# Optimization experiments

Measured on AMD Instinct MI355X. Metric: run time of the kernel, lower is better.

The kernel has to match this reference:

```python
import jax, jax.numpy as jnp
import numpy as np

B, H, N, D = 1, 8, 2048, 64  # n >> d: fastmax's intended long-seq / small-head-dim regime


def setup_inputs() -> dict:
    key = jax.random.key(0)
    kq, kk, kv, kr = jax.random.split(key, 4)
    q = jax.random.normal(kq, (B, H, N, D), dtype=jnp.float32)
    k = jax.random.normal(kk, (B, H, N, D), dtype=jnp.float32)
    v = jax.random.normal(kv, (B, H, N, D), dtype=jnp.float32)
    rpe_matrix = jax.random.normal(kr, (2 * N - 1, D), dtype=jnp.float32)
    return {"q": q, "k": k, "v": v, "rpe_matrix": rpe_matrix, "mask": 1}


def reference(q, k, v, rpe_matrix, mask):
    # Fastmax: 2nd-order Taylor approximation of softmax attention,
    # weight(i,j) = 1 + s_ij + s_ij^2 / 2 where s_ij = q_i . (k_j) + q_i . rpe[i-j+n-1],
    # normalized by the row-sum, optionally causal (mask).
    b, h, n, d = q.shape
    # content scores: (b,h,n,n)
    s = jnp.einsum('bhid,bhjd->bhij', q, k)
    # RPE scores: project q onto every relative-position embedding, then gather
    # the (i,j) -> i-j+n-1 diagonal structure.  qr: (b,h,n,2n-1)
    qr = jnp.einsum('bhid,md->bhim', q, rpe_matrix)
    i = jnp.arange(n)[:, None]
    j = jnp.arange(n)[None, :]
    rel = i - j + (n - 1)  # (n,n) in [0, 2n-2]
    s = s + jnp.take_along_axis(qr, rel[None, None], axis=-1)
    # Taylor-2 exp approximation
    w = 1.0 + s + 0.5 * s * s
    if mask:  # causal
        w = jnp.where(j <= i, w, 0.0)
    denom = jnp.sum(w, axis=-1, keepdims=True)  # (b,h,n,1)
    out = jnp.einsum('bhij,bhjd->bhid', w, v) / denom
    return out
```

## Files before the change

kernel.cpp:

```cpp
#include <hip/hip_runtime.h>
#include <hip/hip_bf16.h>

#define HH 8
#define NN 2048
#define DD 64

typedef __attribute__((ext_vector_type(8))) short bf16x8;
typedef __attribute__((ext_vector_type(4))) float f32x4;
typedef __attribute__((ext_vector_type(8))) unsigned short u16x8;
typedef unsigned short ushort_t;

static __device__ __forceinline__ unsigned short f2bf(float x) {
    union { float f; unsigned u; } un; un.f = x;
    unsigned r = un.u + 0x7FFFu + ((un.u >> 16) & 1u);
    return (unsigned short)(r >> 16);
}

#define OFF_Q  0u
#define OFF_K  2097152u
#define OFF_VT 4194304u
#define OFF_R  6291456u
#define OFF_P  6815744u
#define WS_NEED 11272192u

#define NQ4 262144
#define NR4 65520
__global__ void cvt_kernel(const float* __restrict__ q, const float* __restrict__ k,
                           const float* __restrict__ r, ushort_t* __restrict__ ws) {
    int idx = blockIdx.x * 256 + threadIdx.x;
    const float* src; ushort_t* dst; int off;
    if (idx < NQ4) { src = q; dst = (ushort_t*)((char*)ws + OFF_Q); off = idx; }
    else if (idx < 2 * NQ4) { src = k; dst = (ushort_t*)((char*)ws + OFF_K); off = idx - NQ4; }
    else if (idx < 2 * NQ4 + NR4) { src = r; dst = (ushort_t*)((char*)ws + OFF_R); off = idx - 2 * NQ4; }
    else return;
    float4 f = *(const float4*)&src[4 * (size_t)off];
    ushort4 u; u.x = f2bf(f.x); u.y = f2bf(f.y); u.z = f2bf(f.z); u.w = f2bf(f.w);
    *(ushort4*)&dst[4 * (size_t)off] = u;
}

__global__ void vt_kernel(const float* __restrict__ v, ushort_t* __restrict__ ws) {
    __shared__ __align__(16) ushort_t T[64][72];
    ushort_t* vt = (ushort_t*)((char*)ws + OFF_VT);
    const int h = blockIdx.x >> 5;
    const int n0 = (blockIdx.x & 31) * 64;
    const int tid = threadIdx.x;
    const float* vh = v + (size_t)h * NN * DD;
    #pragma unroll
    for (int p = 0; p < 4; ++p) {
        int c = tid + 256 * p;
        int r = c >> 4, dc = (c & 15) << 2;
        float4 f = *(const float4*)&vh[(size_t)(n0 + r) * DD + dc];
        T[dc + 0][r] = f2bf(f.x); T[dc + 1][r] = f2bf(f.y);
        T[dc + 2][r] = f2bf(f.z); T[dc + 3][r] = f2bf(f.w);
    }
    __syncthreads();
    #pragma unroll
    for (int p = 0; p < 2; ++p) {
        int c = tid + 256 * p;
        int d = c >> 3, nn = (c & 7) << 3;
        *(u16x8*)&vt[((size_t)h * 64 + d) * NN + n0 + nn] = *(const u16x8*)&T[d][nn];
    }
}

__global__ __launch_bounds__(256, 2)
void fastmax_main(const ushort_t* __restrict__ wsb, float* __restrict__ outg,
                  float* __restrict__ wsPart)
{
    __shared__ __align__(16) ushort_t Qs[32][72];
    __shared__ __align__(16) ushort_t Ks[64][72];
    __shared__ __align__(16) ushort_t Bs[96][72];
    __shared__ __align__(16) ushort_t Vts[80][72];
    __shared__ __align__(16) float    Ts[4][16][50];
    __shared__ __align__(16) ushort_t Ws[4][16][40];
    __shared__ __align__(16) float    Epi[32][68];

    const ushort_t* qb  = (const ushort_t*)((const char*)wsb + OFF_Q);
    const ushort_t* kb  = (const ushort_t*)((const char*)wsb + OFF_K);
    const ushort_t* vtb = (const ushort_t*)((const char*)wsb + OFF_VT);
    const ushort_t* rb  = (const ushort_t*)((const char*)wsb + OFF_R);

    const int tid = threadIdx.x;
    const int w   = tid >> 6;
    const int l   = tid & 63;
    const int lq  = l >> 4;
    const int ln  = l & 15;
    const int rt  = w & 1;
    const int ch  = w >> 1;

    const int sb     = blockIdx.x & 1;
    const int stream = blockIdx.x >> 1;
    const int head   = stream & 7;
    const int p      = stream >> 3;
    const int tileA  = 63 - p;
    const int njtA   = (tileA >> 1) + 1;
    const int tileB  = p;
    const int njtB   = (tileB >> 1) + 1;

    const ushort_t* qh  = qb  + (size_t)head * NN * DD;
    const ushort_t* kh  = kb  + (size_t)head * NN * DD;
    const ushort_t* vth = vtb + (size_t)head * DD * NN;
    float*          oh  = outg + (size_t)head * NN * DD;

    for (int idx = tid; idx < 16 * 72; idx += 256) {
        int r = idx / 72, c = idx - r * 72;
        Vts[64 + r][c] = (r == 0) ? (ushort_t)0x3F80 : (ushort_t)0;
    }

    const int sw = 16 * rt - 32 * ch + 32;

    for (int tsel = 0; tsel < 2; ++tsel) {
        if (tsel == 1 && sb == 0) break;
        const int tile = tsel ? tileB : tileA;
        const int jlo  = tsel ? 0 : (sb ? 17 : 0);
        const int jhi  = tsel ? njtB : (sb ? njtA : 17);
        const int i0   = tile * 32;

        __syncthreads();
        { int r = tid >> 3, dc = (tid & 7) << 3;
          *(u16x8*)&Qs[r][dc] = *(const u16x8*)&qh[(size_t)(i0 + r) * DD + dc]; }
        __syncthreads();

        bf16x8 qf0 = *(const bf16x8*)&Qs[16 * rt + ln][ 0 + 8 * lq];
        bf16x8 qf1 = *(const bf16x8*)&Qs[16 * rt + ln][32 + 8 * lq];
        bf16x8 vdf = *(const bf16x8*)&Vts[64 + ln][32 * ch + 8 * lq];

        f32x4 acc0 = {0,0,0,0}, acc1 = {0,0,0,0}, acc2 = {0,0,0,0}, acc3 = {0,0,0,0};
        f32x4 accD = {0,0,0,0};

        for (int jt = jlo; jt < jhi; ++jt) {
            const int j0 = jt * 64;
            __syncthreads();

            #pragma unroll
            for (int p2 = 0; p2 < 2; ++p2) {
                int c = tid + 256 * p2; int r = c >> 3, dc = (c & 7) << 3;
                *(u16x8*)&Ks[r][dc] = *(const u16x8*)&kh[(size_t)(j0 + r) * DD + dc];
            }
            const int relbase = i0 - j0 + 1984;
            #pragma unroll
            for (int p2 = 0; p2 < 3; ++p2) {
                int c = tid + 256 * p2; int r = c >> 3, dc = (c & 7) << 3;
                int row = relbase + r; if (row > 4094) row = 4094;
                *(u16x8*)&Bs[r][dc] = *(const u16x8*)&rb[(size_t)row * DD + dc];
            }
            #pragma unroll
            for (int p2 = 0; p2 < 2; ++p2) {
                int c = tid + 256 * p2; int d = c >> 3, nc = (c & 7) << 3;
                *(u16x8*)&Vts[d][nc] = *(const u16x8*)&vth[(size_t)d * NN + j0 + nc];
            }
            __syncthreads();

            f32x4 s0 = {0,0,0,0}, s1 = {0,0,0,0};
            {
                bf16x8 b00 = *(const bf16x8*)&Ks[32 * ch      + ln][ 0 + 8 * lq];
                bf16x8 b01 = *(const bf16x8*)&Ks[32 * ch      + ln][32 + 8 * lq];
                bf16x8 b10 = *(const bf16x8*)&Ks[32 * ch + 16 + ln][ 0 + 8 * lq];
                bf16x8 b11 = *(const bf16x8*)&Ks[32 * ch + 16 + ln][32 + 8 * lq];
                s0 = __builtin_amdgcn_mfma_f32_16x16x32_bf16(qf0, b00, s0, 0, 0, 0);
                s0 = __builtin_amdgcn_mfma_f32_16x16x32_bf16(qf1, b01, s0, 0, 0, 0);
                s1 = __builtin_amdgcn_mfma_f32_16x16x32_bf16(qf0, b10, s1, 0, 0, 0);
                s1 = __builtin_amdgcn_mfma_f32_16x16x32_bf16(qf1, b11, s1, 0, 0, 0);
            }

            #pragma unroll
            for (int bt = 0; bt < 3; ++bt) {
                f32x4 t = {0,0,0,0};
                bf16x8 b0 = *(const bf16x8*)&Bs[sw + 16 * bt + ln][ 0 + 8 * lq];
                bf16x8 b1 = *(const bf16x8*)&Bs[sw + 16 * bt + ln][32 + 8 * lq];
                t = __builtin_amdgcn_mfma_f32_16x16x32_bf16(qf0, b0, t, 0, 0, 0);
                t = __builtin_amdgcn_mfma_f32_16x16x32_bf16(qf1, b1, t, 0, 0, 0);
                #pragma unroll
                for (int e = 0; e < 4; ++e)
                    Ts[w][4 * lq + e][16 * bt + ln] = t[e];
            }

            #pragma unroll
            for (int ct = 0; ct < 2; ++ct) {
                f32x4 sv = ct ? s1 : s0;
                #pragma unroll
                for (int e = 0; e < 4; ++e) {
                    int rp = 4 * lq + e;
                    int cp = 16 * ct + ln;
                    int bw = rp - cp + 31;
                    float s = sv[e] + Ts[w][rp][bw];
                    float wv = 1.0f + s + 0.5f * s * s;
                    if (j0 + 32 * ch + cp > i0 + 16 * rt + rp) wv = 0.0f;
                    Ws[w][rp][cp] = f2bf(wv);
                }
            }

            {
                bf16x8 af = *(const bf16x8*)&Ws[w][ln][8 * lq];
                bf16x8 b;
                b = *(const bf16x8*)&Vts[ 0 + ln][32 * ch + 8 * lq];
                acc0 = __builtin_amdgcn_mfma_f32_16x16x32_bf16(af, b, acc0, 0, 0, 0);
                b = *(const bf16x8*)&Vts[16 + ln][32 * ch + 8 * lq];
                acc1 = __builtin_amdgcn_mfma_f32_16x16x32_bf16(af, b, acc1, 0, 0, 0);
                b = *(const bf16x8*)&Vts[32 + ln][32 * ch + 8 * lq];
                acc2 = __builtin_amdgcn_mfma_f32_16x16x32_bf16(af, b, acc2, 0, 0, 0);
                b = *(const bf16x8*)&Vts[48 + ln][32 * ch + 8 * lq];
                acc3 = __builtin_amdgcn_mfma_f32_16x16x32_bf16(af, b, acc3, 0, 0, 0);
                accD = __builtin_amdgcn_mfma_f32_16x16x32_bf16(af, vdf, accD, 0, 0, 0);
            }
        }

        __syncthreads();
        if (ch == 0) {
            #pragma unroll
            for (int e = 0; e < 4; ++e) {
                int r = 16 * rt + 4 * lq + e;
                Epi[r][ 0 + ln] = acc0[e];
                Epi[r][16 + ln] = acc1[e];
                Epi[r][32 + ln] = acc2[e];
                Epi[r][48 + ln] = acc3[e];
                if (ln == 0) Epi[r][64] = accD[e];
            }
        }
        __syncthreads();
        if (ch == 1) {
            #pragma unroll
            for (int e = 0; e < 4; ++e) {
                int r = 16 * rt + 4 * lq + e;
                Epi[r][ 0 + ln] += acc0[e];
                Epi[r][16 + ln] += acc1[e];
                Epi[r][32 + ln] += acc2[e];
                Epi[r][48 + ln] += acc3[e];
                if (ln == 0) Epi[r][64] += accD[e];
            }
        }
        __syncthreads();
        if (tsel == 0) {
            float* dst = wsPart + ((size_t)(head * 32 + p) * 2 + sb) * (32 * 68);
            for (int idx = tid; idx < 32 * 68; idx += 256) dst[idx] = (&Epi[0][0])[idx];
        } else {
            #pragma unroll
            for (int e2 = 0; e2 < 8; ++e2) {
                int idx = tid + 256 * e2;
                int r = idx >> 6, d = idx & 63;
                oh[(size_t)(i0 + r) * DD + d] = Epi[r][d] / Epi[r][64];
            }
        }
    }
}

__global__ void combine_kernel(const float* __restrict__ wsPart, float* __restrict__ outg) {
    const int blk = blockIdx.x;
    const int head = blk >> 5;
    const int p = blk & 31;
    const int tileA = 63 - p;
    const float* p0 = wsPart + (size_t)blk * 2 * (32 * 68);
    const float* p1 = p0 + 32 * 68;
    float* oh = outg + (size_t)head * NN * DD;
    #pragma unroll
    for (int e2 = 0; e2 < 8; ++e2) {
        int idx = threadIdx.x + 256 * e2;
        int r = idx >> 6, d = idx & 63;
        float num = p0[r * 68 + d] + p1[r * 68 + d];
        float den = p0[r * 68 + 64] + p1[r * 68 + 64];
        oh[(size_t)(tileA * 32 + r) * DD + d] = num / den;
    }
}

__global__ __launch_bounds__(256, 2)
void fastmax_fallback(const float* __restrict__ qg0, const float* __restrict__ kg0,
                      const float* __restrict__ vg0, const float* __restrict__ rg,
                      float* __restrict__ outg)
{
    __shared__ __align__(16) ushort_t Qs[32][72];
    __shared__ __align__(16) ushort_t Ks[64][72];
    __shared__ __align__(16) ushort_t Bs[96][72];
    __shared__ __align__(16) ushort_t Vts[96][72];
    __shared__ __align__(16) float    Tsf[32][97];
    __shared__ __align__(16) ushort_t Wsf[32][72];
    __shared__ float denomLds[32];

    const int tid = threadIdx.x;
    const int w = tid >> 6, l = tid & 63, lq = l >> 4, ln = l & 15;
    const int head = blockIdx.x & 7, ib = blockIdx.x >> 3;
    const int it = 63 - ib, i0 = it * 32, njt = (it >> 1) + 1;
    const float* qg = qg0 + (size_t)head * NN * DD;
    const float* kg = kg0 + (size_t)head * NN * DD;
    const float* vg = vg0 + (size_t)head * NN * DD;
    float* og = outg + (size_t)head * NN * DD;
    {
        #pragma unroll
        for (int p = 0; p < 2; ++p) {
            int c = tid + 256 * p; int r = c >> 4, dc = (c & 15) << 2;
            float4 f = *(const float4*)&qg[(size_t)(i0 + r) * DD + dc];
            ushort4 u; u.x = f2bf(f.x); u.y = f2bf(f.y); u.z = f2bf(f.z); u.w = f2bf(f.w);
            *(ushort4*)&Qs[r][dc] = u;
        }
        for (int idx = tid; idx < 32 * 72; idx += 256) {
            int rr = idx / 72, cc = idx - rr * 72;
            Vts[64 + rr][cc] = (rr == 0) ? (ushort_t)0x3F80 : (ushort_t)0;
        }
    }
    f32x4 a0 = {0,0,0,0}, a1 = {0,0,0,0}, a2 = {0,0,0,0};
    const int pr = w & 1, rt = w & 1, cp = w >> 1;
    for (int jt = 0; jt < njt; ++jt) {
        const int j0 = jt * 64;
        __syncthreads();
        #pragma unroll
        for (int p = 0; p < 4; ++p) {
            int c = tid + 256 * p; int r = c >> 4, dc = (c & 15) << 2;
            float4 f = *(const float4*)&kg[(size_t)(j0 + r) * DD + dc];
            ushort4 u; u.x = f2bf(f.x); u.y = f2bf(f.y); u.z = f2bf(f.z); u.w = f2bf(f.w);
            *(ushort4*)&Ks[r][dc] = u;
        }
        const int relbase = i0 - j0 + 1984;
        #pragma unroll
        for (int p = 0; p < 6; ++p) {
            int c = tid + 256 * p; int r = c >> 4, dc = (c & 15) << 2;
            int row = relbase + r; if (row > 4094) row = 4094;
            float4 f = *(const float4*)&rg[(size_t)row * DD + dc];
            ushort4 u; u.x = f2bf(f.x); u.y = f2bf(f.y); u.z = f2bf(f.z); u.w = f2bf(f.w);
            *(ushort4*)&Bs[r][dc] = u;
        }
        #pragma unroll
        for (int p = 0; p < 4; ++p) {
            int c = tid + 256 * p; int r = c >> 4, dc = (c & 15) << 2;
            float4 f = *(const float4*)&vg[(size_t)(j0 + r) * DD + dc];
            Vts[dc + 0][r] = f2bf(f.x); Vts[dc + 1][r] = f2bf(f.y);
            Vts[dc + 2][r] = f2bf(f.z); Vts[dc + 3][r] = f2bf(f.w);
        }
        __syncthreads();
        f32x4 s0 = {0,0,0,0}, s1 = {0,0,0,0};
        #pragma unroll
        for (int ks = 0; ks < 2; ++ks) {
            bf16x8 a = *(const bf16x8*)&Qs[16 * rt + ln][32 * ks + 8 * lq];
            bf16x8 b0 = *(const bf16x8*)&Ks[32 * cp + ln][32 * ks + 8 * lq];
            bf16x8 b1 = *(const bf16x8*)&Ks[32 * cp + 16 + ln][32 * ks + 8 * lq];
            s0 = __builtin_amdgcn_mfma_f32_16x16x32_bf16(a, b0, s0, 0, 0, 0);
            s1 = __builtin_amdgcn_mfma_f32_16x16x32_bf16(a, b1, s1, 0, 0, 0);
        }
        #pragma unroll
        for (int kk = 0; kk < 3; ++kk) {
            int bt = (w >> 1) + 2 * kk;
            f32x4 t = {0,0,0,0};
            #pragma unroll
            for (int ks = 0; ks < 2; ++ks) {
                bf16x8 a = *(const bf16x8*)&Qs[16 * rt + ln][32 * ks + 8 * lq];
                bf16x8 b = *(const bf16x8*)&Bs[16 * bt + ln][32 * ks + 8 * lq];
                t = __builtin_amdgcn_mfma_f32_16x16x32_bf16(a, b, t, 0, 0, 0);
            }
            #pragma unroll
            for (int e = 0; e < 4; ++e) Tsf[16 * rt + 4 * lq + e][16 * bt + ln] = t[e];
        }
        __syncthreads();
        #pragma unroll
        for (int ct2 = 0; ct2 < 2; ++ct2) {
            f32x4 sv = ct2 ? s1 : s0;
            int c_loc = 32 * cp + 16 * ct2 + ln, j = j0 + c_loc;
            #pragma unroll
            for (int e = 0; e < 4; ++e) {
                int r_loc = 16 * rt + 4 * lq + e, i = i0 + r_loc;
                float s = sv[e] + Tsf[r_loc][r_loc - c_loc + 63];
                float wv = 1.0f + s + 0.5f * s * s;
                if (j > i) wv = 0.0f;
                Wsf[r_loc][c_loc] = f2bf(wv);
            }
        }
        __syncthreads();
        {
            bf16x8 af0 = *(const bf16x8*)&Wsf[16 * pr + ln][ 0 + 8 * lq];
            bf16x8 af1 = *(const bf16x8*)&Wsf[16 * pr + ln][32 + 8 * lq];
            int pn0 = w >> 1; bf16x8 b;
            b = *(const bf16x8*)&Vts[16 * (pn0 + 0) + ln][ 0 + 8 * lq];
            a0 = __builtin_amdgcn_mfma_f32_16x16x32_bf16(af0, b, a0, 0, 0, 0);
            b = *(const bf16x8*)&Vts[16 * (pn0 + 0) + ln][32 + 8 * lq];
            a0 = __builtin_amdgcn_mfma_f32_16x16x32_bf16(af1, b, a0, 0, 0, 0);
            b = *(const bf16x8*)&Vts[16 * (pn0 + 2) + ln][ 0 + 8 * lq];
            a1 = __builtin_amdgcn_mfma_f32_16x16x32_bf16(af0, b, a1, 0, 0, 0);
            b = *(const bf16x8*)&Vts[16 * (pn0 + 2) + ln][32 + 8 * lq];
            a1 = __builtin_amdgcn_mfma_f32_16x16x32_bf16(af1, b, a1, 0, 0, 0);
            b = *(const bf16x8*)&Vts[16 * (pn0 + 4) + ln][ 0 + 8 * lq];
            a2 = __builtin_amdgcn_mfma_f32_16x16x32_bf16(af0, b, a2, 0, 0, 0);
            b = *(const bf16x8*)&Vts[16 * (pn0 + 4) + ln][32 + 8 * lq];
            a2 = __builtin_amdgcn_mfma_f32_16x16x32_bf16(af1, b, a2, 0, 0, 0);
        }
    }
    if (w < 2 && ln == 0) {
        #pragma unroll
        for (int e = 0; e < 4; ++e) denomLds[16 * pr + 4 * lq + e] = a2[e];
    }
    __syncthreads();
    #pragma unroll
    for (int k = 0; k < 2; ++k) {
        int pn = (w >> 1) + 2 * k;
        f32x4 acc = k ? a1 : a0;
        #pragma unroll
        for (int e = 0; e < 4; ++e) {
            int r_loc = 16 * pr + 4 * lq + e;
            og[(size_t)(i0 + r_loc) * DD + 16 * pn + ln] = acc[e] / denomLds[r_loc];
        }
    }
}

extern "C" void kernel_launch(void* const* d_in, const int* in_sizes, int n_in,
                              void* d_out, int out_size, void* d_ws, size_t ws_size,
                              hipStream_t stream) {
    const float* q   = (const float*)d_in[0];
    const float* k   = (const float*)d_in[1];
    const float* v   = (const float*)d_in[2];
    const float* rpe = (const float*)d_in[3];
    float* out = (float*)d_out;

    if (ws_size >= WS_NEED) {
        ushort_t* wsb = (ushort_t*)d_ws;
        float* wsPart = (float*)((char*)d_ws + OFF_P);
        hipLaunchKernelGGL(cvt_kernel, dim3((2 * NQ4 + NR4 + 255) / 256), dim3(256), 0, stream,
                           q, k, rpe, wsb);
        hipLaunchKernelGGL(vt_kernel, dim3(256), dim3(256), 0, stream, v, wsb);
        hipLaunchKernelGGL(fastmax_main, dim3(512), dim3(256), 0, stream,
                           wsb, out, wsPart);
        hipLaunchKernelGGL(combine_kernel, dim3(256), dim3(256), 0, stream, wsPart, out);
    } else {
        hipLaunchKernelGGL(fastmax_fallback, dim3(512), dim3(256), 0, stream,
                           q, k, v, rpe, out);
    }
}
```

Measured before the change: 107.1 us.

## Split paired causal tiles into three balanced work units, fuse preprocessing kernels

Merges the q/k/rpe conversion and V-transpose kernels into one launch. The main kernel now splits each paired (short+long) query tile stream into three equal segments of 11 key tiles across a 2D grid of 768 blocks, always writing partials that a wider combine kernel reduces over up to three pieces. LDS use is cut by storing the RPE score tile in bf16 and aliasing it with the epilogue buffer, allowing three blocks per CU. This trades extra partial-sum traffic and some bf16 precision loss on the RPE term for better load balance and occupancy.

```diff
diff --git a/kernel.cpp b/kernel.cpp
--- a/kernel.cpp
+++ b/kernel.cpp
@@ -14,6 +14,10 @@
     union { float f; unsigned u; } un; un.f = x;
     unsigned r = un.u + 0x7FFFu + ((un.u >> 16) & 1u);
     return (unsigned short)(r >> 16);
+}
+static __device__ __forceinline__ float bf2f(unsigned short u) {
+    union { unsigned u; float f; } un; un.u = ((unsigned)u) << 16;
+    return un.f;
 }
 
 #define OFF_Q  0u
@@ -21,58 +25,60 @@
 #define OFF_VT 4194304u
 #define OFF_R  6291456u
 #define OFF_P  6815744u
-#define WS_NEED 11272192u
+#define WS_NEED (OFF_P + 256u*3u*2u*32u*68u*4u)
 
 #define NQ4 262144
 #define NR4 65520
-__global__ void cvt_kernel(const float* __restrict__ q, const float* __restrict__ k,
-                           const float* __restrict__ r, ushort_t* __restrict__ ws) {
-    int idx = blockIdx.x * 256 + threadIdx.x;
-    const float* src; ushort_t* dst; int off;
-    if (idx < NQ4) { src = q; dst = (ushort_t*)((char*)ws + OFF_Q); off = idx; }
-    else if (idx < 2 * NQ4) { src = k; dst = (ushort_t*)((char*)ws + OFF_K); off = idx - NQ4; }
-    else if (idx < 2 * NQ4 + NR4) { src = r; dst = (ushort_t*)((char*)ws + OFF_R); off = idx - 2 * NQ4; }
-    else return;
-    float4 f = *(const float4*)&src[4 * (size_t)off];
-    ushort4 u; u.x = f2bf(f.x); u.y = f2bf(f.y); u.z = f2bf(f.z); u.w = f2bf(f.w);
-    *(ushort4*)&dst[4 * (size_t)off] = u;
-}
-
-__global__ void vt_kernel(const float* __restrict__ v, ushort_t* __restrict__ ws) {
+#define CVT_BLOCKS 2305
+__global__ void pre_kernel(const float* __restrict__ q, const float* __restrict__ k,
+                           const float* __restrict__ r, const float* __restrict__ v,
+                           ushort_t* __restrict__ ws) {
     __shared__ __align__(16) ushort_t T[64][72];
-    ushort_t* vt = (ushort_t*)((char*)ws + OFF_VT);
-    const int h = blockIdx.x >> 5;
-    const int n0 = (blockIdx.x & 31) * 64;
-    const int tid = threadIdx.x;
-    const float* vh = v + (size_t)h * NN * DD;
-    #pragma unroll
-    for (int p = 0; p < 4; ++p) {
-        int c = tid + 256 * p;
-        int r = c >> 4, dc = (c & 15) << 2;
-        float4 f = *(const float4*)&vh[(size_t)(n0 + r) * DD + dc];
-        T[dc + 0][r] = f2bf(f.x); T[dc + 1][r] = f2bf(f.y);
-        T[dc + 2][r] = f2bf(f.z); T[dc + 3][r] = f2bf(f.w);
-    }
-    __syncthreads();
-    #pragma unroll
-    for (int p = 0; p < 2; ++p) {
-        int c = tid + 256 * p;
-        int d = c >> 3, nn = (c & 7) << 3;
-        *(u16x8*)&vt[((size_t)h * 64 + d) * NN + n0 + nn] = *(const u16x8*)&T[d][nn];
-    }
-}
-
-__global__ __launch_bounds__(256, 2)
-void fastmax_main(const ushort_t* __restrict__ wsb, float* __restrict__ outg,
-                  float* __restrict__ wsPart)
+    if (blockIdx.x < CVT_BLOCKS) {
+        int idx = blockIdx.x * 256 + threadIdx.x;
+        const float* src; ushort_t* dst; int off;
+        if (idx < NQ4) { src = q; dst = (ushort_t*)((char*)ws + OFF_Q); off = idx; }
+        else if (idx < 2 * NQ4) { src = k; dst = (ushort_t*)((char*)ws + OFF_K); off = idx - NQ4; }
+        else if (idx < 2 * NQ4 + NR4) { src = r; dst = (ushort_t*)((char*)ws + OFF_R); off = idx - 2 * NQ4; }
+        else return;
+        float4 f = *(const float4*)&src[4 * (size_t)off];
+        ushort4 u; u.x = f2bf(f.x); u.y = f2bf(f.y); u.z = f2bf(f.z); u.w = f2bf(f.w);
+        *(ushort4*)&dst[4 * (size_t)off] = u;
+    } else {
+        ushort_t* vt = (ushort_t*)((char*)ws + OFF_VT);
+        const int bb = blockIdx.x - CVT_BLOCKS;
+        const int h = bb >> 5;
+        const int n0 = (bb & 31) * 64;
+        const int tid = threadIdx.x;
+        const float* vh = v + (size_t)h * NN * DD;
+        #pragma unroll
+        for (int p = 0; p < 4; ++p) {
+            int c = tid + 256 * p; int rr = c >> 4, dc = (c & 15) << 2;
+            float4 f = *(const float4*)&vh[(size_t)(n0 + rr) * DD + dc];
+            T[dc + 0][rr] = f2bf(f.x); T[dc + 1][rr] = f2bf(f.y);
+            T[dc + 2][rr] = f2bf(f.z); T[dc + 3][rr] = f2bf(f.w);
+        }
+        __syncthreads();
+        #pragma unroll
+        for (int p = 0; p < 2; ++p) {
+            int c = tid + 256 * p; int d = c >> 3, nn = (c & 7) << 3;
+            *(u16x8*)&vt[((size_t)h * 64 + d) * NN + n0 + nn] = *(const u16x8*)&T[d][nn];
+        }
+    }
+}
+
+__global__ __launch_bounds__(256, 3)
+void fastmax_main(const ushort_t* __restrict__ wsb, float* __restrict__ wsPart)
 {
     __shared__ __align__(16) ushort_t Qs[32][72];
     __shared__ __align__(16) ushort_t Ks[64][72];
     __shared__ __align__(16) ushort_t Bs[96][72];
     __shared__ __align__(16) ushort_t Vts[80][72];
-    __shared__ __align__(16) float    Ts[4][16][50];
-    __shared__ __align__(16) ushort_t Ws[4][16][40];
-    __shared__ __align__(16) float    Epi[32][68];
+    __shared__ __align__(16) unsigned char U[11776];
+
+    ushort_t* TsP = (ushort_t*)U;
+    ushort_t* WsP = (ushort_t*)(U + 6656);
+    float*    Epi = (float*)U;
 
     const ushort_t* qb  = (const ushort_t*)((const char*)wsb + OFF_Q);
     const ushort_t* kb  = (const ushort_t*)((const char*)wsb + OFF_K);
@@ -87,19 +93,19 @@
     const int rt  = w & 1;
     const int ch  = w >> 1;
 
-    const int sb     = blockIdx.x & 1;
-    const int stream = blockIdx.x >> 1;
+    const int stream = blockIdx.x;
+    const int sub    = blockIdx.y;
     const int head   = stream & 7;
     const int p      = stream >> 3;
     const int tileA  = 63 - p;
     const int njtA   = (tileA >> 1) + 1;
     const int tileB  = p;
-    const int njtB   = (tileB >> 1) + 1;
+    const int njtB   = (p >> 1) + 1;
+    const int u0     = 11 * sub, u1 = u0 + 11;
 
     const ushort_t* qh  = qb  + (size_t)head * NN * DD;
     const ushort_t* kh  = kb  + (size_t)head * NN * DD;
     const ushort_t* vth = vtb + (size_t)head * DD * NN;
-    float*          oh  = outg + (size_t)head * NN * DD;
 
     for (int idx = tid; idx < 16 * 72; idx += 256) {
         int r = idx / 72, c = idx - r * 72;
@@ -108,12 +114,20 @@
 
     const int sw = 16 * rt - 32 * ch + 32;
 
-    for (int tsel = 0; tsel < 2; ++tsel) {
-        if (tsel == 1 && sb == 0) break;
-        const int tile = tsel ? tileB : tileA;
-        const int jlo  = tsel ? 0 : (sb ? 17 : 0);
-        const int jhi  = tsel ? njtB : (sb ? njtA : 17);
-        const int i0   = tile * 32;
+    #pragma unroll 1
+    for (int seg = 0; seg < 2; ++seg) {
+        int tile, jlo, jhi, role;
+        if (seg == 0) {
+            tile = tileB; role = 0;
+            jlo = u0; jhi = (u1 < njtB) ? u1 : njtB;
+        } else {
+            tile = tileA; role = 1;
+            int a0 = (u0 > njtB) ? u0 : njtB;
+            jlo = a0 - njtB; jhi = u1 - njtB;
+            if (jhi > njtA) jhi = njtA;
+        }
+        if (jlo >= jhi) continue;
+        const int i0 = tile * 32;
 
         __syncthreads();
         { int r = tid >> 3, dc = (tid & 7) << 3;
@@ -171,7 +185,7 @@
                 t = __builtin_amdgcn_mfma_f32_16x16x32_bf16(qf1, b1, t, 0, 0, 0);
                 #pragma unroll
                 for (int e = 0; e < 4; ++e)
-                    Ts[w][4 * lq + e][16 * bt + ln] = t[e];
+                    TsP[(w * 16 + 4 * lq + e) * 52 + 16 * bt + ln] = f2bf(t[e]);
             }
 
             #pragma unroll
@@ -182,15 +196,15 @@
                     int rp = 4 * lq + e;
                     int cp = 16 * ct + ln;
                     int bw = rp - cp + 31;
-                    float s = sv[e] + Ts[w][rp][bw];
+                    float s = sv[e] + bf2f(TsP[(w * 16 + rp) * 52 + bw]);
                     float wv = 1.0f + s + 0.5f * s * s;
                     if (j0 + 32 * ch + cp > i0 + 16 * rt + rp) wv = 0.0f;
-                    Ws[w][rp][cp] = f2bf(wv);
+                    WsP[(w * 16 + rp) * 40 + cp] = f2bf(wv);
                 }
             }
 
             {
-                bf16x8 af = *(const bf16x8*)&Ws[w][ln][8 * lq];
+                bf16x8 af = *(const bf16x8*)&WsP[(w * 16 + ln) * 40 + 8 * lq];
                 bf16x8 b;
                 b = *(const bf16x8*)&Vts[ 0 + ln][32 * ch + 8 * lq];
                 acc0 = __builtin_amdgcn_mfma_f32_16x16x32_bf16(af, b, acc0, 0, 0, 0);
@@ -209,11 +223,11 @@
             #pragma unroll
             for (int e = 0; e < 4; ++e) {
                 int r = 16 * rt + 4 * lq + e;
-                Epi[r][ 0 + ln] = acc0[e];
-                Epi[r][16 + ln] = acc1[e];
-                Epi[r][32 + ln] = acc2[e];
-                Epi[r][48 + ln] = acc3[e];
-                if (ln == 0) Epi[r][64] = accD[e];
+                Epi[r * 68 +  0 + ln] = acc0[e];
+                Epi[r * 68 + 16 + ln] = acc1[e];
+                Epi[r * 68 + 32 + ln] = acc2[e];
+                Epi[r * 68 + 48 + ln] = acc3[e];
+                if (ln == 0) Epi[r * 68 + 64] = accD[e];
             }
         }
         __syncthreads();
@@ -221,43 +235,46 @@
             #pragma unroll
             for (int e = 0; e < 4; ++e) {
                 int r = 16 * rt + 4 * lq + e;
-                Epi[r][ 0 + ln] += acc0[e];
-                Epi[r][16 + ln] += acc1[e];
-                Epi[r][32 + ln] += acc2[e];
-                Epi[r][48 + ln] += acc3[e];
-                if (ln == 0) Epi[r][64] += accD[e];
-            }
-        }
-        __syncthreads();
-        if (tsel == 0) {
-            float* dst = wsPart + ((size_t)(head * 32 + p) * 2 + sb) * (32 * 68);
-            for (int idx = tid; idx < 32 * 68; idx += 256) dst[idx] = (&Epi[0][0])[idx];
-        } else {
-            #pragma unroll
-            for (int e2 = 0; e2 < 8; ++e2) {
-                int idx = tid + 256 * e2;
-                int r = idx >> 6, d = idx & 63;
-                oh[(size_t)(i0 + r) * DD + d] = Epi[r][d] / Epi[r][64];
-            }
+                Epi[r * 68 +  0 + ln] += acc0[e];
+                Epi[r * 68 + 16 + ln] += acc1[e];
+                Epi[r * 68 + 32 + ln] += acc2[e];
+                Epi[r * 68 + 48 + ln] += acc3[e];
+                if (ln == 0) Epi[r * 68 + 64] += accD[e];
+            }
+        }
+        __syncthreads();
+        {
+            float* dst = wsPart + ((size_t)((stream * 3 + sub) * 2 + role)) * (32 * 68);
+            for (int idx = tid; idx < 32 * 68; idx += 256) dst[idx] = Epi[idx];
         }
     }
 }
 
 __global__ void combine_kernel(const float* __restrict__ wsPart, float* __restrict__ outg) {
-    const int blk = blockIdx.x;
-    const int head = blk >> 5;
-    const int p = blk & 31;
-    const int tileA = 63 - p;
-    const float* p0 = wsPart + (size_t)blk * 2 * (32 * 68);
-    const float* p1 = p0 + 32 * 68;
+    const int c = blockIdx.x;
+    const int head = c >> 6;
+    const int t = c & 63;
+    const int p = (t < 63 - t) ? t : 63 - t;
+    const int role = (t == p) ? 0 : 1;
+    const int stream = p * 8 + head;
+    const int njtB = (p >> 1) + 1;
+    const float* P[3]; int nP = 0;
+    #pragma unroll
+    for (int s = 0; s < 3; ++s) {
+        bool valid = role ? (11 * s + 11 > njtB) : (11 * s < njtB);
+        if (valid) P[nP++] = wsPart + ((size_t)((stream * 3 + s) * 2 + role)) * (32 * 68);
+    }
     float* oh = outg + (size_t)head * NN * DD;
     #pragma unroll
     for (int e2 = 0; e2 < 8; ++e2) {
         int idx = threadIdx.x + 256 * e2;
         int r = idx >> 6, d = idx & 63;
-        float num = p0[r * 68 + d] + p1[r * 68 + d];
-        float den = p0[r * 68 + 64] + p1[r * 68 + 64];
-        oh[(size_t)(tileA * 32 + r) * DD + d] = num / den;
+        float num = 0.f, den = 0.f;
+        for (int s = 0; s < nP; ++s) {
+            num += P[s][r * 68 + d];
+            den += P[s][r * 68 + 64];
+        }
+        oh[(size_t)(t * 32 + r) * DD + d] = num / den;
     }
 }
 
@@ -408,12 +425,10 @@
     if (ws_size >= WS_NEED) {
         ushort_t* wsb = (ushort_t*)d_ws;
         float* wsPart = (float*)((char*)d_ws + OFF_P);
-        hipLaunchKernelGGL(cvt_kernel, dim3((2 * NQ4 + NR4 + 255) / 256), dim3(256), 0, stream,
-                           q, k, rpe, wsb);
-        hipLaunchKernelGGL(vt_kernel, dim3(256), dim3(256), 0, stream, v, wsb);
-        hipLaunchKernelGGL(fastmax_main, dim3(512), dim3(256), 0, stream,
-                           wsb, out, wsPart);
-        hipLaunchKernelGGL(combine_kernel, dim3(256), dim3(256), 0, stream, wsPart, out);
+        hipLaunchKernelGGL(pre_kernel, dim3(CVT_BLOCKS + 256), dim3(256), 0, stream,
+                           q, k, rpe, v, wsb);
+        hipLaunchKernelGGL(fastmax_main, dim3(256, 3), dim3(256), 0, stream, wsb, wsPart);
+        hipLaunchKernelGGL(combine_kernel, dim3(512), dim3(256), 0, stream, wsPart, out);
     } else {
         hipLaunchKernelGGL(fastmax_fallback, dim3(512), dim3(256), 0, stream,
                            q, k, v, rpe, out);
```

Result: slower. 111.8 us (+4.4%).

## Merge preprocessing kernels, load Q fragments directly, compute denominator via shuffles

Applied to the files above, without the earlier changes.

Folds the bf16 conversion kernel and the V-transpose kernel into a single pre_kernel launch, which removes one kernel launch. The main kernel now reads Q MFMA fragments straight from global memory, so the Qs shared tile and its two barriers are gone. The row-sum denominator was an extra MFMA against a ones row kept in shared memory; it is now accumulated in scalar registers from the rounded bf16 weights and reduced with cross-lane shuffles. This trims shared memory and MFMA work, but adds per-element VALU adds and shuffle reductions.

```diff
diff --git a/kernel.cpp b/kernel.cpp
--- a/kernel.cpp
+++ b/kernel.cpp
@@ -14,6 +14,10 @@
     union { float f; unsigned u; } un; un.f = x;
     unsigned r = un.u + 0x7FFFu + ((un.u >> 16) & 1u);
     return (unsigned short)(r >> 16);
+}
+static __device__ __forceinline__ float bf2f(unsigned short u) {
+    union { unsigned u; float f; } un; un.u = ((unsigned)u) << 16;
+    return un.f;
 }
 
 #define OFF_Q  0u
@@ -25,40 +29,41 @@
 
 #define NQ4 262144
 #define NR4 65520
-__global__ void cvt_kernel(const float* __restrict__ q, const float* __restrict__ k,
-                           const float* __restrict__ r, ushort_t* __restrict__ ws) {
-    int idx = blockIdx.x * 256 + threadIdx.x;
-    const float* src; ushort_t* dst; int off;
-    if (idx < NQ4) { src = q; dst = (ushort_t*)((char*)ws + OFF_Q); off = idx; }
-    else if (idx < 2 * NQ4) { src = k; dst = (ushort_t*)((char*)ws + OFF_K); off = idx - NQ4; }
-    else if (idx < 2 * NQ4 + NR4) { src = r; dst = (ushort_t*)((char*)ws + OFF_R); off = idx - 2 * NQ4; }
-    else return;
-    float4 f = *(const float4*)&src[4 * (size_t)off];
-    ushort4 u; u.x = f2bf(f.x); u.y = f2bf(f.y); u.z = f2bf(f.z); u.w = f2bf(f.w);
-    *(ushort4*)&dst[4 * (size_t)off] = u;
-}
-
-__global__ void vt_kernel(const float* __restrict__ v, ushort_t* __restrict__ ws) {
+#define CVT_BLOCKS 2305
+__global__ void pre_kernel(const float* __restrict__ q, const float* __restrict__ k,
+                           const float* __restrict__ r, const float* __restrict__ v,
+                           ushort_t* __restrict__ ws) {
     __shared__ __align__(16) ushort_t T[64][72];
-    ushort_t* vt = (ushort_t*)((char*)ws + OFF_VT);
-    const int h = blockIdx.x >> 5;
-    const int n0 = (blockIdx.x & 31) * 64;
-    const int tid = threadIdx.x;
-    const float* vh = v + (size_t)h * NN * DD;
-    #pragma unroll
-    for (int p = 0; p < 4; ++p) {
-        int c = tid + 256 * p;
-        int r = c >> 4, dc = (c & 15) << 2;
-        float4 f = *(const float4*)&vh[(size_t)(n0 + r) * DD + dc];
-        T[dc + 0][r] = f2bf(f.x); T[dc + 1][r] = f2bf(f.y);
-        T[dc + 2][r] = f2bf(f.z); T[dc + 3][r] = f2bf(f.w);
-    }
-    __syncthreads();
-    #pragma unroll
-    for (int p = 0; p < 2; ++p) {
-        int c = tid + 256 * p;
-        int d = c >> 3, nn = (c & 7) << 3;
-        *(u16x8*)&vt[((size_t)h * 64 + d) * NN + n0 + nn] = *(const u16x8*)&T[d][nn];
+    if (blockIdx.x < CVT_BLOCKS) {
+        int idx = blockIdx.x * 256 + threadIdx.x;
+        const float* src; ushort_t* dst; int off;
+        if (idx < NQ4) { src = q; dst = (ushort_t*)((char*)ws + OFF_Q); off = idx; }
+        else if (idx < 2 * NQ4) { src = k; dst = (ushort_t*)((char*)ws + OFF_K); off = idx - NQ4; }
+        else if (idx < 2 * NQ4 + NR4) { src = r; dst = (ushort_t*)((char*)ws + OFF_R); off = idx - 2 * NQ4; }
+        else return;
+        float4 f = *(const float4*)&src[4 * (size_t)off];
+        ushort4 u; u.x = f2bf(f.x); u.y = f2bf(f.y); u.z = f2bf(f.z); u.w = f2bf(f.w);
+        *(ushort4*)&dst[4 * (size_t)off] = u;
+    } else {
+        ushort_t* vt = (ushort_t*)((char*)ws + OFF_VT);
+        const int bb = blockIdx.x - CVT_BLOCKS;
+        const int h = bb >> 5;
+        const int n0 = (bb & 31) * 64;
+        const int tid = threadIdx.x;
+        const float* vh = v + (size_t)h * NN * DD;
+        #pragma unroll
+        for (int p = 0; p < 4; ++p) {
+            int c = tid + 256 * p; int rr = c >> 4, dc = (c & 15) << 2;
+            float4 f = *(const float4*)&vh[(size_t)(n0 + rr) * DD + dc];
+            T[dc + 0][rr] = f2bf(f.x); T[dc + 1][rr] = f2bf(f.y);
+            T[dc + 2][rr] = f2bf(f.z); T[dc + 3][rr] = f2bf(f.w);
+        }
+        __syncthreads();
+        #pragma unroll
+        for (int p = 0; p < 2; ++p) {
+            int c = tid + 256 * p; int d = c >> 3, nn = (c & 7) << 3;
+            *(u16x8*)&vt[((size_t)h * 64 + d) * NN + n0 + nn] = *(const u16x8*)&T[d][nn];
+        }
     }
 }
 
@@ -66,10 +71,9 @@
 void fastmax_main(const ushort_t* __restrict__ wsb, float* __restrict__ outg,
                   float* __restrict__ wsPart)
 {
-    __shared__ __align__(16) ushort_t Qs[32][72];
     __shared__ __align__(16) ushort_t Ks[64][72];
     __shared__ __align__(16) ushort_t Bs[96][72];
-    __shared__ __align__(16) ushort_t Vts[80][72];
+    __shared__ __align__(16) ushort_t Vts[64][72];
     __shared__ __align__(16) float    Ts[4][16][50];
     __shared__ __align__(16) ushort_t Ws[4][16][40];
     __shared__ __align__(16) float    Epi[32][68];
@@ -101,13 +105,9 @@
     const ushort_t* vth = vtb + (size_t)head * DD * NN;
     float*          oh  = outg + (size_t)head * NN * DD;
 
-    for (int idx = tid; idx < 16 * 72; idx += 256) {
-        int r = idx / 72, c = idx - r * 72;
-        Vts[64 + r][c] = (r == 0) ? (ushort_t)0x3F80 : (ushort_t)0;
-    }
-
     const int sw = 16 * rt - 32 * ch + 32;
 
+    #pragma unroll 1
     for (int tsel = 0; tsel < 2; ++tsel) {
         if (tsel == 1 && sb == 0) break;
         const int tile = tsel ? tileB : tileA;
@@ -115,17 +115,11 @@
         const int jhi  = tsel ? njtB : (sb ? njtA : 17);
         const int i0   = tile * 32;
 
-        __syncthreads();
-        { int r = tid >> 3, dc = (tid & 7) << 3;
-          *(u16x8*)&Qs[r][dc] = *(const u16x8*)&qh[(size_t)(i0 + r) * DD + dc]; }
-        __syncthreads();
-
-        bf16x8 qf0 = *(const bf16x8*)&Qs[16 * rt + ln][ 0 + 8 * lq];
-        bf16x8 qf1 = *(const bf16x8*)&Qs[16 * rt + ln][32 + 8 * lq];
-        bf16x8 vdf = *(const bf16x8*)&Vts[64 + ln][32 * ch + 8 * lq];
+        bf16x8 qf0 = *(const bf16x8*)&qh[(size_t)(i0 + 16 * rt + ln) * DD +  0 + 8 * lq];
+        bf16x8 qf1 = *(const bf16x8*)&qh[(size_t)(i0 + 16 * rt + ln) * DD + 32 + 8 * lq];
 
         f32x4 acc0 = {0,0,0,0}, acc1 = {0,0,0,0}, acc2 = {0,0,0,0}, acc3 = {0,0,0,0};
-        f32x4 accD = {0,0,0,0};
+        float denv0 = 0.f, denv1 = 0.f, denv2 = 0.f, denv3 = 0.f;
 
         for (int jt = jlo; jt < jhi; ++jt) {
             const int j0 = jt * 64;
@@ -185,7 +179,11 @@
                     float s = sv[e] + Ts[w][rp][bw];
                     float wv = 1.0f + s + 0.5f * s * s;
                     if (j0 + 32 * ch + cp > i0 + 16 * rt + rp) wv = 0.0f;
-                    Ws[w][rp][cp] = f2bf(wv);
+                    ushort_t wb = f2bf(wv);
+                    Ws[w][rp][cp] = wb;
+                    float wr = bf2f(wb);
+                    if (e == 0) denv0 += wr; else if (e == 1) denv1 += wr;
+                    else if (e == 2) denv2 += wr; else denv3 += wr;
                 }
             }
 
@@ -200,8 +198,15 @@
                 acc2 = __builtin_amdgcn_mfma_f32_16x16x32_bf16(af, b, acc2, 0, 0, 0);
                 b = *(const bf16x8*)&Vts[48 + ln][32 * ch + 8 * lq];
                 acc3 = __builtin_amdgcn_mfma_f32_16x16x32_bf16(af, b, acc3, 0, 0, 0);
-                accD = __builtin_amdgcn_mfma_f32_16x16x32_bf16(af, vdf, accD, 0, 0, 0);
-            }
+            }
+        }
+
+        #pragma unroll
+        for (int off = 1; off <= 8; off <<= 1) {
+            denv0 += __shfl_xor(denv0, off);
+            denv1 += __shfl_xor(denv1, off);
+            denv2 += __shfl_xor(denv2, off);
+            denv3 += __shfl_xor(denv3, off);
         }
 
         __syncthreads();
@@ -209,11 +214,18 @@
             #pragma unroll
             for (int e = 0; e < 4; ++e) {
                 int r = 16 * rt + 4 * lq + e;
+                f32x4 a = (e == 0) ? acc0 : acc0;
+                (void)a;
                 Epi[r][ 0 + ln] = acc0[e];
                 Epi[r][16 + ln] = acc1[e];
                 Epi[r][32 + ln] = acc2[e];
                 Epi[r][48 + ln] = acc3[e];
-                if (ln == 0) Epi[r][64] = accD[e];
+            }
+            if (ln == 0) {
+                Epi[16 * rt + 4 * lq + 0][64] = denv0;
+                Epi[16 * rt + 4 * lq + 1][64] = denv1;
+                Epi[16 * rt + 4 * lq + 2][64] = denv2;
+                Epi[16 * rt + 4 * lq + 3][64] = denv3;
             }
         }
         __syncthreads();
@@ -225,7 +237,12 @@
                 Epi[r][16 + ln] += acc1[e];
                 Epi[r][32 + ln] += acc2[e];
                 Epi[r][48 + ln] += acc3[e];
-                if (ln == 0) Epi[r][64] += accD[e];
+            }
+            if (ln == 0) {
+                Epi[16 * rt + 4 * lq + 0][64] += denv0;
+                Epi[16 * rt + 4 * lq + 1][64] += denv1;
+                Epi[16 * rt + 4 * lq + 2][64] += denv2;
+                Epi[16 * rt + 4 * lq + 3][64] += denv3;
             }
         }
         __syncthreads();
@@ -267,9 +284,9 @@
                       float* __restrict__ outg)
 {
     __shared__ __align__(16) ushort_t Qs[32][72];
-    __shared__ __align__(16) ushort_t Ks[64][72];
-    __shared__ __align__(16) ushort_t Bs[96][72];
-    __shared__ __align__(16) ushort_t Vts[96][72];
+    __shared__ __align__(16) ushort_t Ks2[64][72];
+    __shared__ __align__(16) ushort_t Bs2[96][72];
+    __shared__ __align__(16) ushort_t Vts2[96][72];
     __shared__ __align__(16) float    Tsf[32][97];
     __shared__ __align__(16) ushort_t Wsf[32][72];
     __shared__ float denomLds[32];
@@ -292,7 +309,7 @@
         }
         for (int idx = tid; idx < 32 * 72; idx += 256) {
             int rr = idx / 72, cc = idx - rr * 72;
-            Vts[64 + rr][cc] = (rr == 0) ? (ushort_t)0x3F80 : (ushort_t)0;
+            Vts2[64 + rr][cc] = (rr == 0) ? (ushort_t)0x3F80 : (ushort_t)0;
         }
     }
     f32x4 a0 = {0,0,0,0}, a1 = {0,0,0,0}, a2 = {0,0,0,0};
@@ -305,7 +322,7 @@
             int c = tid + 256 * p; int r = c >> 4, dc = (c & 15) << 2;
             float4 f = *(const float4*)&kg[(size_t)(j0 + r) * DD + dc];
             ushort4 u; u.x = f2bf(f.x); u.y = f2bf(f.y); u.z = f2bf(f.z); u.w = f2bf(f.w);
-            *(ushort4*)&Ks[r][dc] = u;
+            *(ushort4*)&Ks2[r][dc] = u;
         }
         const int relbase = i0 - j0 + 1984;
         #pragma unroll
@@ -314,22 +331,22 @@
             int row = relbase + r; if (row > 4094) row = 4094;
             float4 f = *(const float4*)&rg[(size_t)row * DD + dc];
             ushort4 u; u.x = f2bf(f.x); u.y = f2bf(f.y); u.z = f2bf(f.z); u.w = f2bf(f.w);
-            *(ushort4*)&Bs[r][dc] = u;
+            *(ushort4*)&Bs2[r][dc] = u;
         }
         #pragma unroll
         for (int p = 0; p < 4; ++p) {
             int c = tid + 256 * p; int r = c >> 4, dc = (c & 15) << 2;
             float4 f = *(const float4*)&vg[(size_t)(j0 + r) * DD + dc];
-            Vts[dc + 0][r] = f2bf(f.x); Vts[dc + 1][r] = f2bf(f.y);
-            Vts[dc + 2][r] = f2bf(f.z); Vts[dc + 3][r] = f2bf(f.w);
+            Vts2[dc + 0][r] = f2bf(f.x); Vts2[dc + 1][r] = f2bf(f.y);
+            Vts2[dc + 2][r] = f2bf(f.z); Vts2[dc + 3][r] = f2bf(f.w);
         }
         __syncthreads();
         f32x4 s0 = {0,0,0,0}, s1 = {0,0,0,0};
         #pragma unroll
         for (int ks = 0; ks < 2; ++ks) {
             bf16x8 a = *(const bf16x8*)&Qs[16 * rt + ln][32 * ks + 8 * lq];
-            bf16x8 b0 = *(const bf16x8*)&Ks[32 * cp + ln][32 * ks + 8 * lq];
-            bf16x8 b1 = *(const bf16x8*)&Ks[32 * cp + 16 + ln][32 * ks + 8 * lq];
+            bf16x8 b0 = *(const bf16x8*)&Ks2[32 * cp + ln][32 * ks + 8 * lq];
+            bf16x8 b1 = *(const bf16x8*)&Ks2[32 * cp + 16 + ln][32 * ks + 8 * lq];
             s0 = __builtin_amdgcn_mfma_f32_16x16x32_bf16(a, b0, s0, 0, 0, 0);
             s1 = __builtin_amdgcn_mfma_f32_16x16x32_bf16(a, b1, s1, 0, 0, 0);
         }
@@ -340,7 +357,7 @@
             #pragma unroll
             for (int ks = 0; ks < 2; ++ks) {
                 bf16x8 a = *(const bf16x8*)&Qs[16 * rt + ln][32 * ks + 8 * lq];
-                bf16x8 b = *(const bf16x8*)&Bs[16 * bt + ln][32 * ks + 8 * lq];
+                bf16x8 b = *(const bf16x8*)&Bs2[16 * bt + ln][32 * ks + 8 * lq];
                 t = __builtin_amdgcn_mfma_f32_16x16x32_bf16(a, b, t, 0, 0, 0);
             }
             #pragma unroll
@@ -365,17 +382,17 @@
             bf16x8 af0 = *(const bf16x8*)&Wsf[16 * pr + ln][ 0 + 8 * lq];
             bf16x8 af1 = *(const bf16x8*)&Wsf[16 * pr + ln][32 + 8 * lq];
             int pn0 = w >> 1; bf16x8 b;
-            b = *(const bf16x8*)&Vts[16 * (pn0 + 0) + ln][ 0 + 8 * lq];
+            b = *(const bf16x8*)&Vts2[16 * (pn0 + 0) + ln][ 0 + 8 * lq];
             a0 = __builtin_amdgcn_mfma_f32_16x16x32_bf16(af0, b, a0, 0, 0, 0);
-            b = *(const bf16x8*)&Vts[16 * (pn0 + 0) + ln][32 + 8 * lq];
+            b = *(const bf16x8*)&Vts2[16 * (pn0 + 0) + ln][32 + 8 * lq];
             a0 = __builtin_amdgcn_mfma_f32_16x16x32_bf16(af1, b, a0, 0, 0, 0);
-            b = *(const bf16x8*)&Vts[16 * (pn0 + 2) + ln][ 0 + 8 * lq];
+            b = *(const bf16x8*)&Vts2[16 * (pn0 + 2) + ln][ 0 + 8 * lq];
             a1 = __builtin_amdgcn_mfma_f32_16x16x32_bf16(af0, b, a1, 0, 0, 0);
-            b = *(const bf16x8*)&Vts[16 * (pn0 + 2) + ln][32 + 8 * lq];
+            b = *(const bf16x8*)&Vts2[16 * (pn0 + 2) + ln][32 + 8 * lq];
             a1 = __builtin_amdgcn_mfma_f32_16x16x32_bf16(af1, b, a1, 0, 0, 0);
-            b = *(const bf16x8*)&Vts[16 * (pn0 + 4) + ln][ 0 + 8 * lq];
+            b = *(const bf16x8*)&Vts2[16 * (pn0 + 4) + ln][ 0 + 8 * lq];
             a2 = __builtin_amdgcn_mfma_f32_16x16x32_bf16(af0, b, a2, 0, 0, 0);
-            b = *(const bf16x8*)&Vts[16 * (pn0 + 4) + ln][32 + 8 * lq];
+            b = *(const bf16x8*)&Vts2[16 * (pn0 + 4) + ln][32 + 8 * lq];
             a2 = __builtin_amdgcn_mfma_f32_16x16x32_bf16(af1, b, a2, 0, 0, 0);
         }
     }
@@ -408,9 +425,8 @@
     if (ws_size >= WS_NEED) {
         ushort_t* wsb = (ushort_t*)d_ws;
         float* wsPart = (float*)((char*)d_ws + OFF_P);
-        hipLaunchKernelGGL(cvt_kernel, dim3((2 * NQ4 + NR4 + 255) / 256), dim3(256), 0, stream,
-                           q, k, rpe, wsb);
-        hipLaunchKernelGGL(vt_kernel, dim3(256), dim3(256), 0, stream, v, wsb);
+        hipLaunchKernelGGL(pre_kernel, dim3(CVT_BLOCKS + 256), dim3(256), 0, stream,
+                           q, k, rpe, v, wsb);
         hipLaunchKernelGGL(fastmax_main, dim3(512), dim3(256), 0, stream,
                            wsb, out, wsPart);
         hipLaunchKernelGGL(combine_kernel, dim3(256), dim3(256), 0, stream, wsPart, out);
```

Measured after the change: 106.1 us. Within noise of the previous version (-0.9%).
